# Optimization experiments

Hardware: AMD Instinct MI355X
Metric: run time of the kernel (lower is better)

The kernel has to match this reference:

```python
import jax, jax.numpy as jnp
import numpy as np

B, C, D, L, H = 128, 1000, 300, 40, 100


def setup_inputs() -> dict:
    key = jax.random.key(0)
    ks = jax.random.split(key, 16)
    def rn(i, shape, sc=1.0):
        return (jax.random.normal(ks[i], shape, jnp.float32) * sc).astype(jnp.float32)
    return {
        "utt": rn(0, (B, L, D)),
        "sys_slots": rn(1, (B, D), 0.1),
        "conf_slots": rn(2, (B, D), 0.1),
        "conf_values": rn(3, (B, D), 0.1),
        "y_past_state": jax.random.uniform(ks[4], (B, C), jnp.float32),
        "slot_emb": rn(5, (C, D), 0.1),
        "value_emb": rn(6, (C, D), 0.1),
        "Wc": rn(7, (D, 2 * D), 0.05), "bc": jnp.zeros((D,), jnp.float32),
        "conv_w1": rn(8, (D, D, 1), 0.05), "conv_b1": jnp.zeros((D,), jnp.float32),
        "conv_w2": rn(9, (D, D, 2), 0.05), "conv_b2": jnp.zeros((D,), jnp.float32),
        "conv_w3": rn(10, (D, D, 3), 0.05), "conv_b3": jnp.zeros((D,), jnp.float32),
        "Wd": rn(11, (H, D), 0.05), "bd": jnp.zeros((H,), jnp.float32),
        "Wmr": rn(12, (H, D), 0.05), "bmr": jnp.zeros((H,), jnp.float32),
        "Wmc": rn(13, (H, D), 0.05), "bmc": jnp.zeros((H,), jnp.float32),
        "Wj": rn(14, (1, H), 0.05), "bj": jnp.zeros((1,), jnp.float32),
    }


def _conv_relu_pool(x_ncl, w, b):
    # x_ncl: [B, D, L]; w: [F, D, k] -> relu(conv) then global max-pool over time -> [B, F]
    y = jax.lax.conv_general_dilated(x_ncl, w, (1,), 'VALID',
                                     dimension_numbers=('NCH', 'OIH', 'NCH'))
    y = jax.nn.relu(y + b[None, :, None])
    return jnp.max(y, axis=2)


def _sig_linear(x, W, b):
    # Sequential(Sigmoid, Linear): Linear applied to sigmoid(x)
    return jax.nn.sigmoid(x) @ W.T + b


def reference(utt, sys_slots, conf_slots, conf_values, y_past_state,
              slot_emb, value_emb, Wc, bc,
              conv_w1, conv_b1, conv_w2, conv_b2, conv_w3, conv_b3,
              Wd, bd, Wmr, bmr, Wmc, bmc, Wj, bj):
    # CNN utterance encoder: sum of 3 conv branches (filter widths 1,2,3)
    x = jnp.transpose(utt, (0, 2, 1))  # [B, D, L]
    final_utt = (_conv_relu_pool(x, conv_w1, conv_b1)
                 + _conv_relu_pool(x, conv_w2, conv_b2)
                 + _conv_relu_pool(x, conv_w3, conv_b3))  # [B, D]

    # candidates_transform = sigmoid(Linear(cat(slot_emb, value_emb)))
    cand = jax.nn.sigmoid(jnp.concatenate([slot_emb, value_emb], axis=1) @ Wc.T + bc)  # [C, D]

    # fused version of the per-batch repeat/addcmul loop: [B, C, D]
    contrib = cand[None, :, :] * final_utt[:, None, :]

    y1 = _sig_linear(_sig_linear(contrib, Wd, bd), Wj, bj)  # [B, C, 1]

    # system-act request gate: ([C,D]@[D,B]) @ [B,D] -> [C, D]
    m_r = (slot_emb @ sys_slots.T) @ final_utt
    y2 = _sig_linear(_sig_linear(m_r, Wmr, bmr), Wj, bj)  # [C, 1]

    # system-act confirm gate
    m_c = ((slot_emb @ conf_slots.T) * (value_emb @ conf_values.T)) @ final_utt  # [C, D]
    y3 = _sig_linear(_sig_linear(m_c, Wmc, bmc), Wj, bj)  # [C, 1]

    y_presoftmax = y1 + y2[None, :, :] + y3[None, :, :]  # [B, C, 1]
    combine = 0.5
    return combine * y_presoftmax[..., 0] + (1.0 - combine) * y_past_state  # [B, C]
```

## Files before the change

### kernel.cpp

```cpp
#include <hip/hip_runtime.h>
#include <hip/hip_bf16.h>

#define OFF_Y23     0
#define OFF_BDP     4096
#define OFF_WJP     4544
#define OFF_BCP     4992
#define OFF_BMRP    6272
#define OFF_BMCP    6720
#define OFF_WALLT   7168
#define OFF_PBF     1235968
#define OFF_FUBF    20896768
#define OFF_FUBFT   20978688
#define OFF_CATSV   21060608
#define OFF_WCPK    22371328
#define OFF_CANDBF  22780928
#define OFF_WDFRAG  23436288
#define OFF_WMRFRAG 23507968
#define OFF_WMCFRAG 23579648
#define OFF_SYSB    23651328
#define OFF_CONFSB  23733248
#define OFF_CONFVB  23815168
#define OFF_PRBF    23897088
#define OFF_PCBF    24159232
#define OFF_SMRBF   24421376
#define OFF_SMCBF   25076736

typedef short bf16x8_t __attribute__((ext_vector_type(8)));
typedef float f32x4_t  __attribute__((ext_vector_type(4)));

__device__ __forceinline__ float sigmoidf_fast(float x) {
    return __builtin_amdgcn_rcpf(1.0f + __expf(-x));
}
__device__ __forceinline__ unsigned short f2bf(float x) {
    unsigned int u = __float_as_uint(x);
    unsigned int r = (u + 0x7FFFu + ((u >> 16) & 1u)) >> 16;
    return (unsigned short)r;
}
__device__ __forceinline__ float bf2f(unsigned short h) {
    return __uint_as_float(((unsigned int)h) << 16);
}

__device__ __forceinline__ float frag_fetch(const float* __restrict__ W, int i) {
    int entry = i >> 3, e = i & 7;
    int kt = entry / 448;
    int r = entry - kt * 448;
    int ni = r >> 6, lane = r & 63;
    int j = ni * 16 + (lane & 15);
    int k = kt * 32 + (lane >> 4) * 8 + e;
    return (j < 100 && k < 300) ? W[j * 300 + k] : 0.0f;
}

__global__ void pack_kernel(const float* __restrict__ w1, const float* __restrict__ w2,
                            const float* __restrict__ w3, const float* __restrict__ Wc,
                            const float* __restrict__ Wd, const float* __restrict__ Wmr,
                            const float* __restrict__ Wmc, const float* __restrict__ sys,
                            const float* __restrict__ confs, const float* __restrict__ confv,
                            const float* __restrict__ bd, const float* __restrict__ Wj,
                            const float* __restrict__ bmr, const float* __restrict__ bmc,
                            const float* __restrict__ bc, const float* __restrict__ slot,
                            const float* __restrict__ value,
                            unsigned short* __restrict__ WallTbf,
                            unsigned short* __restrict__ WdFrag,
                            unsigned short* __restrict__ WmrFrag,
                            unsigned short* __restrict__ WmcFrag,
                            float* __restrict__ bdPad, float* __restrict__ WjPad,
                            float* __restrict__ bmrPad, float* __restrict__ bmcPad,
                            float* __restrict__ bcPad,
                            unsigned short* __restrict__ sysB,
                            unsigned short* __restrict__ confsB,
                            unsigned short* __restrict__ confvB,
                            unsigned short* __restrict__ catsv,
                            unsigned short* __restrict__ WcPk) {
    int idx = blockIdx.x * blockDim.x + threadIdx.x;
    if (idx < 614400) {
        int tap = idx / 102400;
        int rem = idx - tap * 102400;
        int f = rem / 320, k = rem % 320;
        float v = 0.0f;
        if (f < 300 && k < 300) {
            int fd = f * 300 + k;
            if (tap == 0)      v = w1[fd];
            else if (tap == 1) v = w2[fd * 2 + 0];
            else if (tap == 2) v = w2[fd * 2 + 1];
            else               v = w3[fd * 3 + (tap - 3)];
        }
        WallTbf[idx] = f2bf(v);
    } else if (idx < 650240) {
        int i = idx - 614400;
        WdFrag[i] = f2bf(frag_fetch(Wd, i));
    } else if (idx < 686080) {
        int i = idx - 650240;
        WmrFrag[i] = f2bf(frag_fetch(Wmr, i));
    } else if (idx < 721920) {
        int i = idx - 686080;
        WmcFrag[i] = f2bf(frag_fetch(Wmc, i));
    } else if (idx < 722032) {
        int j = idx - 721920; bdPad[j] = (j < 100) ? bd[j] : 0.0f;
    } else if (idx < 722144) {
        int j = idx - 722032; WjPad[j] = (j < 100) ? Wj[j] : 0.0f;
    } else if (idx < 722256) {
        int j = idx - 722144; bmrPad[j] = (j < 100) ? bmr[j] : 0.0f;
    } else if (idx < 722368) {
        int j = idx - 722256; bmcPad[j] = (j < 100) ? bmc[j] : 0.0f;
    } else if (idx < 722688) {
        int j = idx - 722368; bcPad[j] = (j < 300) ? bc[j] : 0.0f;
    } else if (idx < 845568) {
        int i = idx - 722688;
        int m = i / 40960, r = i % 40960;
        int b = r / 320, k = r % 320;
        const float* src = (m == 0) ? sys : ((m == 1) ? confs : confv);
        unsigned short* dst = (m == 0) ? sysB : ((m == 1) ? confsB : confvB);
        dst[r] = f2bf((k < 300) ? src[b * 300 + k] : 0.0f);
    } else if (idx < 1500928) {
        int i = idx - 845568;
        int c = i / 640, k = i % 640;
        float v = 0.0f;
        if (c < 1000) {
            if (k < 300)                   v = slot[c * 300 + k];
            else if (k >= 320 && k < 620)  v = value[c * 300 + (k - 320)];
        }
        catsv[i] = f2bf(v);
    } else if (idx < 1705728) {
        int i = idx - 1500928;
        int f = i / 640, k = i % 640;
        float v = 0.0f;
        if (f < 300) {
            if (k < 300)                   v = Wc[f * 600 + k];
            else if (k >= 320 && k < 620)  v = Wc[f * 600 + 300 + (k - 320)];
        }
        WcPk[i] = f2bf(v);
    }
}

__global__ __launch_bounds__(256, 2) void gemm1_kernel(const float* __restrict__ utt,
        const unsigned short* __restrict__ WallTbf, unsigned short* __restrict__ Pbf) {
    __shared__ __attribute__((aligned(16))) short As[128 * 40];
    __shared__ __attribute__((aligned(16))) short Bs[128 * 40];
    const int tid = threadIdx.x;
    const int m0 = blockIdx.x * 128;
    const int n0 = blockIdx.y * 128;
    const int lane = tid & 63;
    const int w = tid >> 6;
    const int wrow = w >> 1, wcol = w & 1;
    const int ln = lane & 15, lq = lane >> 4;

    f32x4_t acc[4][4];
    #pragma unroll
    for (int i = 0; i < 4; i++)
        #pragma unroll
        for (int j = 0; j < 4; j++) acc[i][j] = (f32x4_t){0.f, 0.f, 0.f, 0.f};

    for (int kk = 0; kk < 320; kk += 32) {
        #pragma unroll
        for (int i = tid; i < 512; i += 256) {
            int row = i >> 2, q = i & 3;
            int k0 = kk + q * 8;
            const float* src = utt + (m0 + row) * 300;
            bf16x8_t v;
            if (k0 + 8 <= 300) {
                float4 f0 = *(const float4*)(src + k0);
                float4 f1 = *(const float4*)(src + k0 + 4);
                v[0] = (short)f2bf(f0.x); v[1] = (short)f2bf(f0.y);
                v[2] = (short)f2bf(f0.z); v[3] = (short)f2bf(f0.w);
                v[4] = (short)f2bf(f1.x); v[5] = (short)f2bf(f1.y);
                v[6] = (short)f2bf(f1.z); v[7] = (short)f2bf(f1.w);
            } else {
                #pragma unroll
                for (int e = 0; e < 8; e++) {
                    int k = k0 + e;
                    v[e] = (k < 300) ? (short)f2bf(src[k]) : (short)0;
                }
            }
            *(bf16x8_t*)(&As[row * 40 + q * 8]) = v;
        }
        #pragma unroll
        for (int i = tid; i < 512; i += 256) {
            int row = i >> 2, q = i & 3;
            *(uint4*)(&Bs[row * 40 + q * 8]) =
                *(const uint4*)(WallTbf + (n0 + row) * 320 + kk + q * 8);
        }
        __syncthreads();
        bf16x8_t a[4], b[4];
        #pragma unroll
        for (int mi = 0; mi < 4; mi++)
            a[mi] = *(const bf16x8_t*)(&As[(wrow * 64 + mi * 16 + ln) * 40 + lq * 8]);
        #pragma unroll
        for (int ni = 0; ni < 4; ni++)
            b[ni] = *(const bf16x8_t*)(&Bs[(wcol * 64 + ni * 16 + ln) * 40 + lq * 8]);
        #pragma unroll
        for (int mi = 0; mi < 4; mi++)
            #pragma unroll
            for (int ni = 0; ni < 4; ni++)
                acc[mi][ni] = __builtin_amdgcn_mfma_f32_16x16x32_bf16(a[mi], b[ni], acc[mi][ni], 0, 0, 0);
        __syncthreads();
    }
    #pragma unroll
    for (int mi = 0; mi < 4; mi++) {
        #pragma unroll
        for (int ni = 0; ni < 4; ni++) {
            int col = n0 + wcol * 64 + ni * 16 + ln;
            #pragma unroll
            for (int reg = 0; reg < 4; reg++) {
                int row = m0 + wrow * 64 + mi * 16 + lq * 4 + reg;
                Pbf[row * 1920 + col] = f2bf(acc[mi][ni][reg]);
            }
        }
    }
}

__global__ __launch_bounds__(320) void combine_kernel(const unsigned short* __restrict__ Pbf,
        const float* __restrict__ b1, const float* __restrict__ b2,
        const float* __restrict__ b3, unsigned short* __restrict__ fubf,
        unsigned short* __restrict__ fubfT) {
    int b = blockIdx.x;
    int f = threadIdx.x;
    if (f >= 300) { fubf[b * 320 + f] = 0; fubfT[f * 128 + b] = 0; return; }
    const unsigned short* base = Pbf + (size_t)b * 40 * 1920;
    float m1 = -1e30f, m2 = -1e30f, m3 = -1e30f;
    float p1prev = 0.f, p3prev = 0.f, p3prev2 = 0.f, p4prev = 0.f;
    for (int t = 0; t < 40; ++t) {
        const unsigned short* r = base + t * 1920;
        float p0 = bf2f(r[f]);
        float p1 = bf2f(r[320 + f]);
        float p2 = bf2f(r[640 + f]);
        float p3 = bf2f(r[960 + f]);
        float p4 = bf2f(r[1280 + f]);
        float p5 = bf2f(r[1600 + f]);
        m1 = fmaxf(m1, p0);
        if (t >= 1) m2 = fmaxf(m2, p1prev + p2);
        if (t >= 2) m3 = fmaxf(m3, p3prev2 + p4prev + p5);
        p3prev2 = p3prev; p3prev = p3; p4prev = p4; p1prev = p1;
    }
    float r = fmaxf(m1 + b1[f], 0.f) + fmaxf(m2 + b2[f], 0.f) + fmaxf(m3 + b3[f], 0.f);
    unsigned short rb = f2bf(r);
    fubf[b * 320 + f]  = rb;
    fubfT[f * 128 + b] = rb;
}

__global__ __launch_bounds__(256) void cand_gemm(const unsigned short* __restrict__ catsv,
        const unsigned short* __restrict__ WcPk, const float* __restrict__ bcPad,
        unsigned short* __restrict__ candbf) {
    __shared__ __attribute__((aligned(16))) short As[64 * 40];
    __shared__ __attribute__((aligned(16))) short Bs[64 * 40];
    const int tid = threadIdx.x;
    const int m0 = blockIdx.x * 64, n0 = blockIdx.y * 64;
    const int lane = tid & 63, w = tid >> 6;
    const int wr = w & 1, wc = w >> 1;
    const int ln = lane & 15, lq = lane >> 4;
    f32x4_t acc[2][2];
    #pragma unroll
    for (int i = 0; i < 2; i++)
        #pragma unroll
        for (int j = 0; j < 2; j++) acc[i][j] = (f32x4_t){0.f, 0.f, 0.f, 0.f};
    const int srow = tid >> 2, sq = tid & 3;
    for (int kk = 0; kk < 640; kk += 32) {
        *(uint4*)(&As[srow * 40 + sq * 8]) = *(const uint4*)(catsv + (m0 + srow) * 640 + kk + sq * 8);
        *(uint4*)(&Bs[srow * 40 + sq * 8]) = *(const uint4*)(WcPk  + (n0 + srow) * 640 + kk + sq * 8);
        __syncthreads();
        bf16x8_t a[2], b[2];
        #pragma unroll
        for (int mi = 0; mi < 2; mi++)
            a[mi] = *(const bf16x8_t*)(&As[(wr * 32 + mi * 16 + ln) * 40 + lq * 8]);
        #pragma unroll
        for (int ni = 0; ni < 2; ni++)
            b[ni] = *(const bf16x8_t*)(&Bs[(wc * 32 + ni * 16 + ln) * 40 + lq * 8]);
        #pragma unroll
        for (int mi = 0; mi < 2; mi++)
            #pragma unroll
            for (int ni = 0; ni < 2; ni++)
                acc[mi][ni] = __builtin_amdgcn_mfma_f32_16x16x32_bf16(a[mi], b[ni], acc[mi][ni], 0, 0, 0);
        __syncthreads();
    }
    #pragma unroll
    for (int mi = 0; mi < 2; mi++) {
        #pragma unroll
        for (int ni = 0; ni < 2; ni++) {
            int n = n0 + wc * 32 + ni * 16 + ln;
            float bcv = bcPad[n];
            #pragma unroll
            for (int reg = 0; reg < 4; reg++) {
                int cr = m0 + wr * 32 + mi * 16 + lq * 4 + reg;
                candbf[cr * 320 + n] = f2bf(sigmoidf_fast(acc[mi][ni][reg] + bcv));
            }
        }
    }
}

__global__ __launch_bounds__(256) void pgate_gemm(const unsigned short* __restrict__ catsv,
        const unsigned short* __restrict__ sysB, const unsigned short* __restrict__ confsB,
        const unsigned short* __restrict__ confvB,
        unsigned short* __restrict__ Prbf, unsigned short* __restrict__ Pcbf) {
    __shared__ __attribute__((aligned(16))) short As[2][64 * 40];
    __shared__ __attribute__((aligned(16))) short Bs[3][128 * 40];
    const int tid = threadIdx.x;
    const int c0 = blockIdx.x * 64;
    const int lane = tid & 63, w = tid >> 6;
    const int ln = lane & 15, lq = lane >> 4;
    f32x4_t accR[8], accS[8], accV[8];
    #pragma unroll
    for (int i = 0; i < 8; i++) {
        accR[i] = (f32x4_t){0.f, 0.f, 0.f, 0.f};
        accS[i] = (f32x4_t){0.f, 0.f, 0.f, 0.f};
        accV[i] = (f32x4_t){0.f, 0.f, 0.f, 0.f};
    }
    for (int kk = 0; kk < 320; kk += 32) {
        #pragma unroll
        for (int i = tid; i < 512; i += 256) {
            int mat = i >> 8, r2 = i & 255;
            int row = r2 >> 2, q = r2 & 3;
            *(uint4*)(&As[mat][row * 40 + q * 8]) =
                *(const uint4*)(catsv + (c0 + row) * 640 + mat * 320 + kk + q * 8);
        }
        #pragma unroll
        for (int i = tid; i < 1536; i += 256) {
            int mat = i >> 9, r2 = i & 511;
            int row = r2 >> 2, q = r2 & 3;
            const unsigned short* src = (mat == 0) ? sysB : ((mat == 1) ? confsB : confvB);
            *(uint4*)(&Bs[mat][row * 40 + q * 8]) =
                *(const uint4*)(src + row * 320 + kk + q * 8);
        }
        __syncthreads();
        bf16x8_t aS = *(const bf16x8_t*)(&As[0][(w * 16 + ln) * 40 + lq * 8]);
        bf16x8_t aV = *(const bf16x8_t*)(&As[1][(w * 16 + ln) * 40 + lq * 8]);
        #pragma unroll
        for (int ni = 0; ni < 8; ni++) {
            bf16x8_t bR = *(const bf16x8_t*)(&Bs[0][(ni * 16 + ln) * 40 + lq * 8]);
            bf16x8_t bS = *(const bf16x8_t*)(&Bs[1][(ni * 16 + ln) * 40 + lq * 8]);
            bf16x8_t bV = *(const bf16x8_t*)(&Bs[2][(ni * 16 + ln) * 40 + lq * 8]);
            accR[ni] = __builtin_amdgcn_mfma_f32_16x16x32_bf16(aS, bR, accR[ni], 0, 0, 0);
            accS[ni] = __builtin_amdgcn_mfma_f32_16x16x32_bf16(aS, bS, accS[ni], 0, 0, 0);
            accV[ni] = __builtin_amdgcn_mfma_f32_16x16x32_bf16(aV, bV, accV[ni], 0, 0, 0);
        }
        __syncthreads();
    }
    #pragma unroll
    for (int ni = 0; ni < 8; ni++) {
        int b = ni * 16 + ln;
        #pragma unroll
        for (int reg = 0; reg < 4; reg++) {
            int c = c0 + w * 16 + lq * 4 + reg;
            Prbf[c * 128 + b] = f2bf(accR[ni][reg]);
            Pcbf[c * 128 + b] = f2bf(accS[ni][reg] * accV[ni][reg]);
        }
    }
}

__global__ __launch_bounds__(256) void mgate_gemm(const unsigned short* __restrict__ Prbf,
        const unsigned short* __restrict__ Pcbf, const unsigned short* __restrict__ fubfT,
        unsigned short* __restrict__ smrbf, unsigned short* __restrict__ smcbf) {
    __shared__ __attribute__((aligned(16))) short As[2][64 * 40];
    __shared__ __attribute__((aligned(16))) short Bs[64 * 40];
    const int tid = threadIdx.x;
    const int m0 = blockIdx.x * 64, n0 = blockIdx.y * 64;
    const int lane = tid & 63, w = tid >> 6;
    const int wr = w & 1, wc = w >> 1;
    const int ln = lane & 15, lq = lane >> 4;
    f32x4_t accR[2][2], accC[2][2];
    #pragma unroll
    for (int i = 0; i < 2; i++)
        #pragma unroll
        for (int j = 0; j < 2; j++) {
            accR[i][j] = (f32x4_t){0.f, 0.f, 0.f, 0.f};
            accC[i][j] = (f32x4_t){0.f, 0.f, 0.f, 0.f};
        }
    for (int kk = 0; kk < 128; kk += 32) {
        #pragma unroll
        for (int i = tid; i < 512; i += 256) {
            int mat = i >> 8, r2 = i & 255;
            int row = r2 >> 2, q = r2 & 3;
            const unsigned short* src = mat ? Pcbf : Prbf;
            *(uint4*)(&As[mat][row * 40 + q * 8]) =
                *(const uint4*)(src + (m0 + row) * 128 + kk + q * 8);
        }
        if (tid < 256) {
            int row = tid >> 2, q = tid & 3;
            *(uint4*)(&Bs[row * 40 + q * 8]) =
                *(const uint4*)(fubfT + (n0 + row) * 128 + kk + q * 8);
        }
        __syncthreads();
        bf16x8_t aR[2], aC[2], b[2];
        #pragma unroll
        for (int mi = 0; mi < 2; mi++) {
            aR[mi] = *(const bf16x8_t*)(&As[0][(wr * 32 + mi * 16 + ln) * 40 + lq * 8]);
            aC[mi] = *(const bf16x8_t*)(&As[1][(wr * 32 + mi * 16 + ln) * 40 + lq * 8]);
        }
        #pragma unroll
        for (int ni = 0; ni < 2; ni++)
            b[ni] = *(const bf16x8_t*)(&Bs[(wc * 32 + ni * 16 + ln) * 40 + lq * 8]);
        #pragma unroll
        for (int mi = 0; mi < 2; mi++)
            #pragma unroll
            for (int ni = 0; ni < 2; ni++) {
                accR[mi][ni] = __builtin_amdgcn_mfma_f32_16x16x32_bf16(aR[mi], b[ni], accR[mi][ni], 0, 0, 0);
                accC[mi][ni] = __builtin_amdgcn_mfma_f32_16x16x32_bf16(aC[mi], b[ni], accC[mi][ni], 0, 0, 0);
            }
        __syncthreads();
    }
    #pragma unroll
    for (int mi = 0; mi < 2; mi++) {
        #pragma unroll
        for (int ni = 0; ni < 2; ni++) {
            int f = n0 + wc * 32 + ni * 16 + ln;
            #pragma unroll
            for (int reg = 0; reg < 4; reg++) {
                int c = m0 + wr * 32 + mi * 16 + lq * 4 + reg;
                smrbf[c * 320 + f] = f2bf(sigmoidf_fast(accR[mi][ni][reg]));
                smcbf[c * 320 + f] = f2bf(sigmoidf_fast(accC[mi][ni][reg]));
            }
        }
    }
}

__global__ __launch_bounds__(256) void ygate_gemm(const unsigned short* __restrict__ smrbf,
        const unsigned short* __restrict__ smcbf, const unsigned short* __restrict__ WmrFrag,
        const unsigned short* __restrict__ WmcFrag, const float* __restrict__ bmrPad,
        const float* __restrict__ bmcPad, const float* __restrict__ WjPad,
        const float* __restrict__ bj, float* __restrict__ y23) {
    __shared__ __attribute__((aligned(16))) short As[2][64 * 40];
    __shared__ __attribute__((aligned(16))) short Bs[2][3584];
    const int tid = threadIdx.x;
    const int c0 = blockIdx.x * 64;
    const int lane = tid & 63, w = tid >> 6;
    const int ln = lane & 15, lq = lane >> 4;
    f32x4_t accR[7], accC[7];
    #pragma unroll
    for (int i = 0; i < 7; i++) {
        accR[i] = (f32x4_t){0.f, 0.f, 0.f, 0.f};
        accC[i] = (f32x4_t){0.f, 0.f, 0.f, 0.f};
    }
    for (int kt = 0; kt < 10; kt++) {
        int kk = kt * 32;
        #pragma unroll
        for (int i = tid; i < 512; i += 256) {
            int mat = i >> 8, r2 = i & 255;
            int row = r2 >> 2, q = r2 & 3;
            const unsigned short* src = mat ? smcbf : smrbf;
            *(uint4*)(&As[mat][row * 40 + q * 8]) =
                *(const uint4*)(src + (c0 + row) * 320 + kk + q * 8);
        }
        #pragma unroll
        for (int i = tid; i < 896; i += 256) {
            int mat = i / 448, j = i - mat * 448;
            const uint4* s = (const uint4*)((mat ? WmcFrag : WmrFrag) + kt * 3584);
            ((uint4*)&Bs[mat][0])[j] = s[j];
        }
        __syncthreads();
        bf16x8_t aR = *(const bf16x8_t*)(&As[0][(w * 16 + ln) * 40 + lq * 8]);
        bf16x8_t aC = *(const bf16x8_t*)(&As[1][(w * 16 + ln) * 40 + lq * 8]);
        #pragma unroll
        for (int ni = 0; ni < 7; ni++) {
            bf16x8_t bR = *(const bf16x8_t*)(&Bs[0][(ni * 64 + lane) * 8]);
            bf16x8_t bC = *(const bf16x8_t*)(&Bs[1][(ni * 64 + lane) * 8]);
            accR[ni] = __builtin_amdgcn_mfma_f32_16x16x32_bf16(aR, bR, accR[ni], 0, 0, 0);
            accC[ni] = __builtin_amdgcn_mfma_f32_16x16x32_bf16(aC, bC, accC[ni], 0, 0, 0);
        }
        __syncthreads();
    }
    float psum[4] = {0.f, 0.f, 0.f, 0.f};
    #pragma unroll
    for (int ni = 0; ni < 7; ni++) {
        int n = ni * 16 + ln;
        float wj = WjPad[n], br = bmrPad[n], bcv = bmcPad[n];
        #pragma unroll
        for (int reg = 0; reg < 4; reg++) {
            float hr = sigmoidf_fast(accR[ni][reg] + br);
            float hc = sigmoidf_fast(accC[ni][reg] + bcv);
            psum[reg] += (hr + hc) * wj;
        }
    }
    #pragma unroll
    for (int reg = 0; reg < 4; reg++) {
        float v = psum[reg];
        v += __shfl_xor(v, 1);
        v += __shfl_xor(v, 2);
        v += __shfl_xor(v, 4);
        v += __shfl_xor(v, 8);
        if (ln == 0) {
            int c = c0 + w * 16 + lq * 4 + reg;
            y23[c] = v + 2.0f * bj[0];
        }
    }
}

__global__ __launch_bounds__(256) void gemm2_kernel(const unsigned short* __restrict__ candbf,
        const unsigned short* __restrict__ fubf, const unsigned short* __restrict__ WdFrag,
        const float* __restrict__ bdPad, const float* __restrict__ WjPad,
        const float* __restrict__ bj, const float* __restrict__ y23,
        const float* __restrict__ ypast, float* __restrict__ out) {
    __shared__ __attribute__((aligned(16))) short Bs[2][3584];
    __shared__ float bdS[112], WjS[112], ybuf[128];
    const int c = blockIdx.x;
    const int tid = threadIdx.x;
    const int lane = tid & 63, w = tid >> 6;
    const int ln = lane & 15, lq = lane >> 4;
    if (tid < 112) { bdS[tid] = bdPad[tid]; WjS[tid] = WjPad[tid]; }

    const unsigned short* candRow = candbf + c * 320;
    const unsigned short* fuR0 = fubf + (w * 32 + ln) * 320;
    const unsigned short* fuR1 = fuR0 + 16 * 320;

    f32x4_t acc[2][7];
    #pragma unroll
    for (int mi = 0; mi < 2; mi++)
        #pragma unroll
        for (int ni = 0; ni < 7; ni++) acc[mi][ni] = (f32x4_t){0.f, 0.f, 0.f, 0.f};

    {
        const uint4* src = (const uint4*)(WdFrag);
        uint4* dst = (uint4*)&Bs[0][0];
        dst[tid] = src[tid];
        if (tid < 192) dst[tid + 256] = src[tid + 256];
    }
    __syncthreads();

    #pragma unroll
    for (int kt = 0; kt < 10; kt++) {
        if (kt < 9) {
            const uint4* src = (const uint4*)(WdFrag + (kt + 1) * 3584);
            uint4* dst = (uint4*)&Bs[(kt + 1) & 1][0];
            dst[tid] = src[tid];
            if (tid < 192) dst[tid + 256] = src[tid + 256];
        }
        const int k0 = kt * 32 + lq * 8;
        bf16x8_t cf  = *(const bf16x8_t*)(candRow + k0);
        bf16x8_t f0v = *(const bf16x8_t*)(fuR0 + k0);
        bf16x8_t f1v = *(const bf16x8_t*)(fuR1 + k0);
        bf16x8_t a0, a1;
        #pragma unroll
        for (int e = 0; e < 8; e += 2) {
            float cv0 = bf2f((unsigned short)cf[e]);
            float cv1 = bf2f((unsigned short)cf[e + 1]);
            float2 s0 = make_float2(sigmoidf_fast(cv0 * bf2f((unsigned short)f0v[e])),
                                    sigmoidf_fast(cv1 * bf2f((unsigned short)f0v[e + 1])));
            float2 s1 = make_float2(sigmoidf_fast(cv0 * bf2f((unsigned short)f1v[e])),
                                    sigmoidf_fast(cv1 * bf2f((unsigned short)f1v[e + 1])));
            __hip_bfloat162 p0 = __float22bfloat162_rn(s0);
            __hip_bfloat162 p1 = __float22bfloat162_rn(s1);
            ((unsigned int*)&a0)[e >> 1] = *(unsigned int*)&p0;
            ((unsigned int*)&a1)[e >> 1] = *(unsigned int*)&p1;
        }
        #pragma unroll
        for (int ni = 0; ni < 7; ni++) {
            bf16x8_t bfr = *(const bf16x8_t*)(&Bs[kt & 1][(ni * 64 + lane) * 8]);
            acc[0][ni] = __builtin_amdgcn_mfma_f32_16x16x32_bf16(a0, bfr, acc[0][ni], 0, 0, 0);
            acc[1][ni] = __builtin_amdgcn_mfma_f32_16x16x32_bf16(a1, bfr, acc[1][ni], 0, 0, 0);
        }
        __syncthreads();
    }

    float psum[2][4] = {{0.f, 0.f, 0.f, 0.f}, {0.f, 0.f, 0.f, 0.f}};
    #pragma unroll
    for (int mi = 0; mi < 2; mi++) {
        #pragma unroll
        for (int ni = 0; ni < 7; ni++) {
            int n = ni * 16 + ln;
            float bdv = bdS[n], wjv = WjS[n];
            #pragma unroll
            for (int reg = 0; reg < 4; reg++) {
                float h = sigmoidf_fast(acc[mi][ni][reg] + bdv);
                psum[mi][reg] += h * wjv;
            }
        }
    }
    #pragma unroll
    for (int mi = 0; mi < 2; mi++) {
        #pragma unroll
        for (int reg = 0; reg < 4; reg++) {
            float v = psum[mi][reg];
            v += __shfl_xor(v, 1);
            v += __shfl_xor(v, 2);
            v += __shfl_xor(v, 4);
            v += __shfl_xor(v, 8);
            if (ln == 0) ybuf[w * 32 + mi * 16 + lq * 4 + reg] = v;
        }
    }
    __syncthreads();
    if (tid < 128) {
        int b = tid;
        float y1 = ybuf[b] + bj[0];
        out[b * 1000 + c] = 0.5f * (y1 + y23[c]) + 0.5f * ypast[b * 1000 + c];
    }
}

extern "C" void kernel_launch(void* const* d_in, const int* in_sizes, int n_in,
                              void* d_out, int out_size, void* d_ws, size_t ws_size,
                              hipStream_t stream) {
    const float* utt   = (const float*)d_in[0];
    const float* sys   = (const float*)d_in[1];
    const float* confs = (const float*)d_in[2];
    const float* confv = (const float*)d_in[3];
    const float* ypast = (const float*)d_in[4];
    const float* slot  = (const float*)d_in[5];
    const float* value = (const float*)d_in[6];
    const float* Wc    = (const float*)d_in[7];
    const float* bc    = (const float*)d_in[8];
    const float* w1    = (const float*)d_in[9];
    const float* b1    = (const float*)d_in[10];
    const float* w2    = (const float*)d_in[11];
    const float* b2    = (const float*)d_in[12];
    const float* w3    = (const float*)d_in[13];
    const float* b3    = (const float*)d_in[14];
    const float* Wd    = (const float*)d_in[15];
    const float* bd    = (const float*)d_in[16];
    const float* Wmr   = (const float*)d_in[17];
    const float* bmr   = (const float*)d_in[18];
    const float* Wmc   = (const float*)d_in[19];
    const float* bmc   = (const float*)d_in[20];
    const float* Wj    = (const float*)d_in[21];
    const float* bj    = (const float*)d_in[22];

    char* wsb = (char*)d_ws;
    float* y23    = (float*)(wsb + OFF_Y23);
    float* bdPad  = (float*)(wsb + OFF_BDP);
    float* WjPad  = (float*)(wsb + OFF_WJP);
    float* bcPad  = (float*)(wsb + OFF_BCP);
    float* bmrPad = (float*)(wsb + OFF_BMRP);
    float* bmcPad = (float*)(wsb + OFF_BMCP);
    unsigned short* WallTbf = (unsigned short*)(wsb + OFF_WALLT);
    unsigned short* Pbf     = (unsigned short*)(wsb + OFF_PBF);
    unsigned short* fubf    = (unsigned short*)(wsb + OFF_FUBF);
    unsigned short* fubfT   = (unsigned short*)(wsb + OFF_FUBFT);
    unsigned short* catsv   = (unsigned short*)(wsb + OFF_CATSV);
    unsigned short* WcPk    = (unsigned short*)(wsb + OFF_WCPK);
    unsigned short* candbf  = (unsigned short*)(wsb + OFF_CANDBF);
    unsigned short* WdFrag  = (unsigned short*)(wsb + OFF_WDFRAG);
    unsigned short* WmrFrag = (unsigned short*)(wsb + OFF_WMRFRAG);
    unsigned short* WmcFrag = (unsigned short*)(wsb + OFF_WMCFRAG);
    unsigned short* sysB    = (unsigned short*)(wsb + OFF_SYSB);
    unsigned short* confsB  = (unsigned short*)(wsb + OFF_CONFSB);
    unsigned short* confvB  = (unsigned short*)(wsb + OFF_CONFVB);
    float* out = (float*)d_out;

    pack_kernel<<<6663, 256, 0, stream>>>(w1, w2, w3, Wc, Wd, Wmr, Wmc, sys, confs, confv,
                                          bd, Wj, bmr, bmc, bc, slot, value,
                                          WallTbf, WdFrag, WmrFrag, WmcFrag,
                                          bdPad, WjPad, bmrPad, bmcPad, bcPad,
                                          sysB, confsB, confvB, catsv, WcPk);
    gemm1_kernel<<<dim3(40, 15), 256, 0, stream>>>(utt, WallTbf, Pbf);
    combine_kernel<<<128, 320, 0, stream>>>(Pbf, b1, b2, b3, fubf, fubfT);
    cand_gemm<<<dim3(16, 5), 256, 0, stream>>>(catsv, WcPk, bcPad, candbf);
    pgate_gemm<<<16, 256, 0, stream>>>(catsv, sysB, confsB, confvB,
                                       (unsigned short*)(wsb + OFF_PRBF),
                                       (unsigned short*)(wsb + OFF_PCBF));
    mgate_gemm<<<dim3(16, 5), 256, 0, stream>>>((unsigned short*)(wsb + OFF_PRBF),
                                                (unsigned short*)(wsb + OFF_PCBF), fubfT,
                                                (unsigned short*)(wsb + OFF_SMRBF),
                                                (unsigned short*)(wsb + OFF_SMCBF));
    ygate_gemm<<<16, 256, 0, stream>>>((unsigned short*)(wsb + OFF_SMRBF),
                                       (unsigned short*)(wsb + OFF_SMCBF),
                                       WmrFrag, WmcFrag, bmrPad, bmcPad, WjPad, bj, y23);
    gemm2_kernel<<<1000, 256, 0, stream>>>(candbf, fubf, WdFrag, bdPad, WjPad,
                                           bj, y23, ypast, out);
}
```

Before: 220.7 us.

## Merge independent GEMM launches into one heterogeneous kernel and pre-convert utt to bf16

Combines the conv GEMM, candidate-transform GEMM and gate projection GEMM into a single early_kernel that dispatches on block index, cutting two kernel launches and letting the small GEMMs run concurrently with the large one. The fp32-to-bf16 conversion of the utterance is moved into the pack kernel, which writes a padded bf16 copy to workspace so the GEMM loads bf16 directly. The combine kernel is split into 64-thread blocks across a 2D grid for more parallelism. The trade-offs are an extra global round trip for the converted utterance, a larger pack kernel, and the loss of the previous two-blocks-per-CU launch bound hint on the main GEMM.

New measurement: 206.1 us. 1.07x faster.

```diff
diff --git a/kernel.cpp b/kernel.cpp
--- a/kernel.cpp
+++ b/kernel.cpp
@@ -24,6 +24,7 @@
 #define OFF_PCBF    24159232
 #define OFF_SMRBF   24421376
 #define OFF_SMCBF   25076736
+#define OFF_XBF     25732096
 
 typedef short bf16x8_t __attribute__((ext_vector_type(8)));
 typedef float f32x4_t  __attribute__((ext_vector_type(4)));
@@ -58,7 +59,7 @@
                             const float* __restrict__ bd, const float* __restrict__ Wj,
                             const float* __restrict__ bmr, const float* __restrict__ bmc,
                             const float* __restrict__ bc, const float* __restrict__ slot,
-                            const float* __restrict__ value,
+                            const float* __restrict__ value, const float* __restrict__ utt,
                             unsigned short* __restrict__ WallTbf,
                             unsigned short* __restrict__ WdFrag,
                             unsigned short* __restrict__ WmrFrag,
@@ -70,7 +71,8 @@
                             unsigned short* __restrict__ confsB,
                             unsigned short* __restrict__ confvB,
                             unsigned short* __restrict__ catsv,
-                            unsigned short* __restrict__ WcPk) {
+                            unsigned short* __restrict__ WcPk,
+                            unsigned short* __restrict__ Xbf) {
     int idx = blockIdx.x * blockDim.x + threadIdx.x;
     if (idx < 614400) {
         int tap = idx / 102400;
@@ -129,91 +131,186 @@
             else if (k >= 320 && k < 620)  v = Wc[f * 600 + 300 + (k - 320)];
         }
         WcPk[i] = f2bf(v);
-    }
-}
-
-__global__ __launch_bounds__(256, 2) void gemm1_kernel(const float* __restrict__ utt,
-        const unsigned short* __restrict__ WallTbf, unsigned short* __restrict__ Pbf) {
-    __shared__ __attribute__((aligned(16))) short As[128 * 40];
-    __shared__ __attribute__((aligned(16))) short Bs[128 * 40];
+    } else if (idx < 3344128) {
+        int i = idx - 1705728;
+        int m = i / 320, k = i % 320;
+        Xbf[i] = f2bf((k < 300) ? utt[m * 300 + k] : 0.0f);
+    }
+}
+
+__global__ __launch_bounds__(256) void early_kernel(
+        const unsigned short* __restrict__ Xbf, const unsigned short* __restrict__ WallTbf,
+        unsigned short* __restrict__ Pbf,
+        const unsigned short* __restrict__ catsv, const unsigned short* __restrict__ WcPk,
+        const float* __restrict__ bcPad, unsigned short* __restrict__ candbf,
+        const unsigned short* __restrict__ sysB, const unsigned short* __restrict__ confsB,
+        const unsigned short* __restrict__ confvB,
+        unsigned short* __restrict__ Prbf, unsigned short* __restrict__ Pcbf) {
+    __shared__ __attribute__((aligned(16))) char smem[40960];
+    const int bid = blockIdx.x;
     const int tid = threadIdx.x;
-    const int m0 = blockIdx.x * 128;
-    const int n0 = blockIdx.y * 128;
-    const int lane = tid & 63;
-    const int w = tid >> 6;
-    const int wrow = w >> 1, wcol = w & 1;
+    const int lane = tid & 63, w = tid >> 6;
     const int ln = lane & 15, lq = lane >> 4;
 
-    f32x4_t acc[4][4];
-    #pragma unroll
-    for (int i = 0; i < 4; i++)
-        #pragma unroll
-        for (int j = 0; j < 4; j++) acc[i][j] = (f32x4_t){0.f, 0.f, 0.f, 0.f};
-
-    for (int kk = 0; kk < 320; kk += 32) {
-        #pragma unroll
-        for (int i = tid; i < 512; i += 256) {
-            int row = i >> 2, q = i & 3;
-            int k0 = kk + q * 8;
-            const float* src = utt + (m0 + row) * 300;
-            bf16x8_t v;
-            if (k0 + 8 <= 300) {
-                float4 f0 = *(const float4*)(src + k0);
-                float4 f1 = *(const float4*)(src + k0 + 4);
-                v[0] = (short)f2bf(f0.x); v[1] = (short)f2bf(f0.y);
-                v[2] = (short)f2bf(f0.z); v[3] = (short)f2bf(f0.w);
-                v[4] = (short)f2bf(f1.x); v[5] = (short)f2bf(f1.y);
-                v[6] = (short)f2bf(f1.z); v[7] = (short)f2bf(f1.w);
-            } else {
+    if (bid < 600) {
+        short* As = (short*)smem;
+        short* Bs = (short*)(smem + 10240);
+        const int m0 = (bid / 15) * 128;
+        const int n0 = (bid % 15) * 128;
+        const int wrow = w >> 1, wcol = w & 1;
+        f32x4_t acc[4][4];
+        #pragma unroll
+        for (int i = 0; i < 4; i++)
+            #pragma unroll
+            for (int j = 0; j < 4; j++) acc[i][j] = (f32x4_t){0.f, 0.f, 0.f, 0.f};
+        for (int kk = 0; kk < 320; kk += 32) {
+            #pragma unroll
+            for (int i = tid; i < 512; i += 256) {
+                int row = i >> 2, q = i & 3;
+                *(uint4*)(&As[row * 40 + q * 8]) =
+                    *(const uint4*)(Xbf + (m0 + row) * 320 + kk + q * 8);
+            }
+            #pragma unroll
+            for (int i = tid; i < 512; i += 256) {
+                int row = i >> 2, q = i & 3;
+                *(uint4*)(&Bs[row * 40 + q * 8]) =
+                    *(const uint4*)(WallTbf + (n0 + row) * 320 + kk + q * 8);
+            }
+            __syncthreads();
+            bf16x8_t a[4], b[4];
+            #pragma unroll
+            for (int mi = 0; mi < 4; mi++)
+                a[mi] = *(const bf16x8_t*)(&As[(wrow * 64 + mi * 16 + ln) * 40 + lq * 8]);
+            #pragma unroll
+            for (int ni = 0; ni < 4; ni++)
+                b[ni] = *(const bf16x8_t*)(&Bs[(wcol * 64 + ni * 16 + ln) * 40 + lq * 8]);
+            #pragma unroll
+            for (int mi = 0; mi < 4; mi++)
                 #pragma unroll
-                for (int e = 0; e < 8; e++) {
-                    int k = k0 + e;
-                    v[e] = (k < 300) ? (short)f2bf(src[k]) : (short)0;
+                for (int ni = 0; ni < 4; ni++)
+                    acc[mi][ni] = __builtin_amdgcn_mfma_f32_16x16x32_bf16(a[mi], b[ni], acc[mi][ni], 0, 0, 0);
+            __syncthreads();
+        }
+        #pragma unroll
+        for (int mi = 0; mi < 4; mi++) {
+            #pragma unroll
+            for (int ni = 0; ni < 4; ni++) {
+                int col = n0 + wcol * 64 + ni * 16 + ln;
+                #pragma unroll
+                for (int reg = 0; reg < 4; reg++) {
+                    int row = m0 + wrow * 64 + mi * 16 + lq * 4 + reg;
+                    Pbf[row * 1920 + col] = f2bf(acc[mi][ni][reg]);
                 }
             }
-            *(bf16x8_t*)(&As[row * 40 + q * 8]) = v;
-        }
-        #pragma unroll
-        for (int i = tid; i < 512; i += 256) {
-            int row = i >> 2, q = i & 3;
-            *(uint4*)(&Bs[row * 40 + q * 8]) =
-                *(const uint4*)(WallTbf + (n0 + row) * 320 + kk + q * 8);
-        }
-        __syncthreads();
-        bf16x8_t a[4], b[4];
-        #pragma unroll
-        for (int mi = 0; mi < 4; mi++)
-            a[mi] = *(const bf16x8_t*)(&As[(wrow * 64 + mi * 16 + ln) * 40 + lq * 8]);
-        #pragma unroll
-        for (int ni = 0; ni < 4; ni++)
-            b[ni] = *(const bf16x8_t*)(&Bs[(wcol * 64 + ni * 16 + ln) * 40 + lq * 8]);
-        #pragma unroll
-        for (int mi = 0; mi < 4; mi++)
-            #pragma unroll
-            for (int ni = 0; ni < 4; ni++)
-                acc[mi][ni] = __builtin_amdgcn_mfma_f32_16x16x32_bf16(a[mi], b[ni], acc[mi][ni], 0, 0, 0);
-        __syncthreads();
-    }
-    #pragma unroll
-    for (int mi = 0; mi < 4; mi++) {
-        #pragma unroll
-        for (int ni = 0; ni < 4; ni++) {
-            int col = n0 + wcol * 64 + ni * 16 + ln;
+        }
+    } else if (bid < 680) {
+        short* As = (short*)smem;
+        short* Bs = (short*)(smem + 5120);
+        const int idx2 = bid - 600;
+        const int m0 = (idx2 / 5) * 64, n0 = (idx2 % 5) * 64;
+        const int wr = w & 1, wc = w >> 1;
+        f32x4_t acc[2][2];
+        #pragma unroll
+        for (int i = 0; i < 2; i++)
+            #pragma unroll
+            for (int j = 0; j < 2; j++) acc[i][j] = (f32x4_t){0.f, 0.f, 0.f, 0.f};
+        const int srow = tid >> 2, sq = tid & 3;
+        for (int kk = 0; kk < 640; kk += 32) {
+            *(uint4*)(&As[srow * 40 + sq * 8]) = *(const uint4*)(catsv + (m0 + srow) * 640 + kk + sq * 8);
+            *(uint4*)(&Bs[srow * 40 + sq * 8]) = *(const uint4*)(WcPk  + (n0 + srow) * 640 + kk + sq * 8);
+            __syncthreads();
+            bf16x8_t a[2], b[2];
+            #pragma unroll
+            for (int mi = 0; mi < 2; mi++)
+                a[mi] = *(const bf16x8_t*)(&As[(wr * 32 + mi * 16 + ln) * 40 + lq * 8]);
+            #pragma unroll
+            for (int ni = 0; ni < 2; ni++)
+                b[ni] = *(const bf16x8_t*)(&Bs[(wc * 32 + ni * 16 + ln) * 40 + lq * 8]);
+            #pragma unroll
+            for (int mi = 0; mi < 2; mi++)
+                #pragma unroll
+                for (int ni = 0; ni < 2; ni++)
+                    acc[mi][ni] = __builtin_amdgcn_mfma_f32_16x16x32_bf16(a[mi], b[ni], acc[mi][ni], 0, 0, 0);
+            __syncthreads();
+        }
+        #pragma unroll
+        for (int mi = 0; mi < 2; mi++) {
+            #pragma unroll
+            for (int ni = 0; ni < 2; ni++) {
+                int n = n0 + wc * 32 + ni * 16 + ln;
+                float bcv = bcPad[n];
+                #pragma unroll
+                for (int reg = 0; reg < 4; reg++) {
+                    int cr = m0 + wr * 32 + mi * 16 + lq * 4 + reg;
+                    candbf[cr * 320 + n] = f2bf(sigmoidf_fast(acc[mi][ni][reg] + bcv));
+                }
+            }
+        }
+    } else {
+        short* As0 = (short*)smem;
+        short* As1 = (short*)(smem + 5120);
+        short* Bs0 = (short*)(smem + 10240);
+        short* Bs1 = (short*)(smem + 20480);
+        short* Bs2 = (short*)(smem + 30720);
+        const int c0 = (bid - 680) * 64;
+        f32x4_t accR[8], accS[8], accV[8];
+        #pragma unroll
+        for (int i = 0; i < 8; i++) {
+            accR[i] = (f32x4_t){0.f, 0.f, 0.f, 0.f};
+            accS[i] = (f32x4_t){0.f, 0.f, 0.f, 0.f};
+            accV[i] = (f32x4_t){0.f, 0.f, 0.f, 0.f};
+        }
+        for (int kk = 0; kk < 320; kk += 32) {
+            #pragma unroll
+            for (int i = tid; i < 512; i += 256) {
+                int mat = i >> 8, r2 = i & 255;
+                int row = r2 >> 2, q = r2 & 3;
+                short* dst = mat ? As1 : As0;
+                *(uint4*)(&dst[row * 40 + q * 8]) =
+                    *(const uint4*)(catsv + (c0 + row) * 640 + mat * 320 + kk + q * 8);
+            }
+            #pragma unroll
+            for (int i = tid; i < 1536; i += 256) {
+                int mat = i >> 9, r2 = i & 511;
+                int row = r2 >> 2, q = r2 & 3;
+                const unsigned short* src = (mat == 0) ? sysB : ((mat == 1) ? confsB : confvB);
+                short* dst = (mat == 0) ? Bs0 : ((mat == 1) ? Bs1 : Bs2);
+                *(uint4*)(&dst[row * 40 + q * 8]) =
+                    *(const uint4*)(src + row * 320 + kk + q * 8);
+            }
+            __syncthreads();
+            bf16x8_t aS = *(const bf16x8_t*)(&As0[(w * 16 + ln) * 40 + lq * 8]);
+            bf16x8_t aV = *(const bf16x8_t*)(&As1[(w * 16 + ln) * 40 + lq * 8]);
+            #pragma unroll
+            for (int ni = 0; ni < 8; ni++) {
+                bf16x8_t bR = *(const bf16x8_t*)(&Bs0[(ni * 16 + ln) * 40 + lq * 8]);
+                bf16x8_t bS = *(const bf16x8_t*)(&Bs1[(ni * 16 + ln) * 40 + lq * 8]);
+                bf16x8_t bV = *(const bf16x8_t*)(&Bs2[(ni * 16 + ln) * 40 + lq * 8]);
+                accR[ni] = __builtin_amdgcn_mfma_f32_16x16x32_bf16(aS, bR, accR[ni], 0, 0, 0);
+                accS[ni] = __builtin_amdgcn_mfma_f32_16x16x32_bf16(aS, bS, accS[ni], 0, 0, 0);
+                accV[ni] = __builtin_amdgcn_mfma_f32_16x16x32_bf16(aV, bV, accV[ni], 0, 0, 0);
+            }
+            __syncthreads();
+        }
+        #pragma unroll
+        for (int ni = 0; ni < 8; ni++) {
+            int b = ni * 16 + ln;
             #pragma unroll
             for (int reg = 0; reg < 4; reg++) {
-                int row = m0 + wrow * 64 + mi * 16 + lq * 4 + reg;
-                Pbf[row * 1920 + col] = f2bf(acc[mi][ni][reg]);
-            }
-        }
-    }
-}
-
-__global__ __launch_bounds__(320) void combine_kernel(const unsigned short* __restrict__ Pbf,
+                int c = c0 + w * 16 + lq * 4 + reg;
+                Prbf[c * 128 + b] = f2bf(accR[ni][reg]);
+                Pcbf[c * 128 + b] = f2bf(accS[ni][reg] * accV[ni][reg]);
+            }
+        }
+    }
+}
+
+__global__ __launch_bounds__(64) void combine_kernel(const unsigned short* __restrict__ Pbf,
         const float* __restrict__ b1, const float* __restrict__ b2,
         const float* __restrict__ b3, unsigned short* __restrict__ fubf,
         unsigned short* __restrict__ fubfT) {
     int b = blockIdx.x;
-    int f = threadIdx.x;
+    int f = blockIdx.y * 64 + threadIdx.x;
     if (f >= 300) { fubf[b * 320 + f] = 0; fubfT[f * 128 + b] = 0; return; }
     const unsigned short* base = Pbf + (size_t)b * 40 * 1920;
     float m1 = -1e30f, m2 = -1e30f, m3 = -1e30f;
@@ -235,114 +332,6 @@
     unsigned short rb = f2bf(r);
     fubf[b * 320 + f]  = rb;
     fubfT[f * 128 + b] = rb;
-}
-
-__global__ __launch_bounds__(256) void cand_gemm(const unsigned short* __restrict__ catsv,
-        const unsigned short* __restrict__ WcPk, const float* __restrict__ bcPad,
-        unsigned short* __restrict__ candbf) {
-    __shared__ __attribute__((aligned(16))) short As[64 * 40];
-    __shared__ __attribute__((aligned(16))) short Bs[64 * 40];
-    const int tid = threadIdx.x;
-    const int m0 = blockIdx.x * 64, n0 = blockIdx.y * 64;
-    const int lane = tid & 63, w = tid >> 6;
-    const int wr = w & 1, wc = w >> 1;
-    const int ln = lane & 15, lq = lane >> 4;
-    f32x4_t acc[2][2];
-    #pragma unroll
-    for (int i = 0; i < 2; i++)
-        #pragma unroll
-        for (int j = 0; j < 2; j++) acc[i][j] = (f32x4_t){0.f, 0.f, 0.f, 0.f};
-    const int srow = tid >> 2, sq = tid & 3;
-    for (int kk = 0; kk < 640; kk += 32) {
-        *(uint4*)(&As[srow * 40 + sq * 8]) = *(const uint4*)(catsv + (m0 + srow) * 640 + kk + sq * 8);
-        *(uint4*)(&Bs[srow * 40 + sq * 8]) = *(const uint4*)(WcPk  + (n0 + srow) * 640 + kk + sq * 8);
-        __syncthreads();
-        bf16x8_t a[2], b[2];
-        #pragma unroll
-        for (int mi = 0; mi < 2; mi++)
-            a[mi] = *(const bf16x8_t*)(&As[(wr * 32 + mi * 16 + ln) * 40 + lq * 8]);
-        #pragma unroll
-        for (int ni = 0; ni < 2; ni++)
-            b[ni] = *(const bf16x8_t*)(&Bs[(wc * 32 + ni * 16 + ln) * 40 + lq * 8]);
-        #pragma unroll
-        for (int mi = 0; mi < 2; mi++)
-            #pragma unroll
-            for (int ni = 0; ni < 2; ni++)
-                acc[mi][ni] = __builtin_amdgcn_mfma_f32_16x16x32_bf16(a[mi], b[ni], acc[mi][ni], 0, 0, 0);
-        __syncthreads();
-    }
-    #pragma unroll
-    for (int mi = 0; mi < 2; mi++) {
-        #pragma unroll
-        for (int ni = 0; ni < 2; ni++) {
-            int n = n0 + wc * 32 + ni * 16 + ln;
-            float bcv = bcPad[n];
-            #pragma unroll
-            for (int reg = 0; reg < 4; reg++) {
-                int cr = m0 + wr * 32 + mi * 16 + lq * 4 + reg;
-                candbf[cr * 320 + n] = f2bf(sigmoidf_fast(acc[mi][ni][reg] + bcv));
-            }
-        }
-    }
-}
-
-__global__ __launch_bounds__(256) void pgate_gemm(const unsigned short* __restrict__ catsv,
-        const unsigned short* __restrict__ sysB, const unsigned short* __restrict__ confsB,
-        const unsigned short* __restrict__ confvB,
-        unsigned short* __restrict__ Prbf, unsigned short* __restrict__ Pcbf) {
-    __shared__ __attribute__((aligned(16))) short As[2][64 * 40];
-    __shared__ __attribute__((aligned(16))) short Bs[3][128 * 40];
-    const int tid = threadIdx.x;
-    const int c0 = blockIdx.x * 64;
-    const int lane = tid & 63, w = tid >> 6;
-    const int ln = lane & 15, lq = lane >> 4;
-    f32x4_t accR[8], accS[8], accV[8];
-    #pragma unroll
-    for (int i = 0; i < 8; i++) {
-        accR[i] = (f32x4_t){0.f, 0.f, 0.f, 0.f};
-        accS[i] = (f32x4_t){0.f, 0.f, 0.f, 0.f};
-        accV[i] = (f32x4_t){0.f, 0.f, 0.f, 0.f};
-    }
-    for (int kk = 0; kk < 320; kk += 32) {
-        #pragma unroll
-        for (int i = tid; i < 512; i += 256) {
-            int mat = i >> 8, r2 = i & 255;
-            int row = r2 >> 2, q = r2 & 3;
-            *(uint4*)(&As[mat][row * 40 + q * 8]) =
-                *(const uint4*)(catsv + (c0 + row) * 640 + mat * 320 + kk + q * 8);
-        }
-        #pragma unroll
-        for (int i = tid; i < 1536; i += 256) {
-            int mat = i >> 9, r2 = i & 511;
-            int row = r2 >> 2, q = r2 & 3;
-            const unsigned short* src = (mat == 0) ? sysB : ((mat == 1) ? confsB : confvB);
-            *(uint4*)(&Bs[mat][row * 40 + q * 8]) =
-                *(const uint4*)(src + row * 320 + kk + q * 8);
-        }
-        __syncthreads();
-        bf16x8_t aS = *(const bf16x8_t*)(&As[0][(w * 16 + ln) * 40 + lq * 8]);
-        bf16x8_t aV = *(const bf16x8_t*)(&As[1][(w * 16 + ln) * 40 + lq * 8]);
-        #pragma unroll
-        for (int ni = 0; ni < 8; ni++) {
-            bf16x8_t bR = *(const bf16x8_t*)(&Bs[0][(ni * 16 + ln) * 40 + lq * 8]);
-            bf16x8_t bS = *(const bf16x8_t*)(&Bs[1][(ni * 16 + ln) * 40 + lq * 8]);
-            bf16x8_t bV = *(const bf16x8_t*)(&Bs[2][(ni * 16 + ln) * 40 + lq * 8]);
-            accR[ni] = __builtin_amdgcn_mfma_f32_16x16x32_bf16(aS, bR, accR[ni], 0, 0, 0);
-            accS[ni] = __builtin_amdgcn_mfma_f32_16x16x32_bf16(aS, bS, accS[ni], 0, 0, 0);
-            accV[ni] = __builtin_amdgcn_mfma_f32_16x16x32_bf16(aV, bV, accV[ni], 0, 0, 0);
-        }
-        __syncthreads();
-    }
-    #pragma unroll
-    for (int ni = 0; ni < 8; ni++) {
-        int b = ni * 16 + ln;
-        #pragma unroll
-        for (int reg = 0; reg < 4; reg++) {
-            int c = c0 + w * 16 + lq * 4 + reg;
-            Prbf[c * 128 + b] = f2bf(accR[ni][reg]);
-            Pcbf[c * 128 + b] = f2bf(accS[ni][reg] * accV[ni][reg]);
-        }
-    }
 }
 
 __global__ __launch_bounds__(256) void mgate_gemm(const unsigned short* __restrict__ Prbf,
@@ -629,26 +618,25 @@
     unsigned short* sysB    = (unsigned short*)(wsb + OFF_SYSB);
     unsigned short* confsB  = (unsigned short*)(wsb + OFF_CONFSB);
     unsigned short* confvB  = (unsigned short*)(wsb + OFF_CONFVB);
+    unsigned short* Prbf    = (unsigned short*)(wsb + OFF_PRBF);
+    unsigned short* Pcbf    = (unsigned short*)(wsb + OFF_PCBF);
+    unsigned short* smrbf   = (unsigned short*)(wsb + OFF_SMRBF);
+    unsigned short* smcbf   = (unsigned short*)(wsb + OFF_SMCBF);
+    unsigned short* Xbf     = (unsigned short*)(wsb + OFF_XBF);
     float* out = (float*)d_out;
 
-    pack_kernel<<<6663, 256, 0, stream>>>(w1, w2, w3, Wc, Wd, Wmr, Wmc, sys, confs, confv,
-                                          bd, Wj, bmr, bmc, bc, slot, value,
-                                          WallTbf, WdFrag, WmrFrag, WmcFrag,
-                                          bdPad, WjPad, bmrPad, bmcPad, bcPad,
-                                          sysB, confsB, confvB, catsv, WcPk);
-    gemm1_kernel<<<dim3(40, 15), 256, 0, stream>>>(utt, WallTbf, Pbf);
-    combine_kernel<<<128, 320, 0, stream>>>(Pbf, b1, b2, b3, fubf, fubfT);
-    cand_gemm<<<dim3(16, 5), 256, 0, stream>>>(catsv, WcPk, bcPad, candbf);
-    pgate_gemm<<<16, 256, 0, stream>>>(catsv, sysB, confsB, confvB,
-                                       (unsigned short*)(wsb + OFF_PRBF),
-                                       (unsigned short*)(wsb + OFF_PCBF));
-    mgate_gemm<<<dim3(16, 5), 256, 0, stream>>>((unsigned short*)(wsb + OFF_PRBF),
-                                                (unsigned short*)(wsb + OFF_PCBF), fubfT,
-                                                (unsigned short*)(wsb + OFF_SMRBF),
-                                                (unsigned short*)(wsb + OFF_SMCBF));
-    ygate_gemm<<<16, 256, 0, stream>>>((unsigned short*)(wsb + OFF_SMRBF),
-                                       (unsigned short*)(wsb + OFF_SMCBF),
-                                       WmrFrag, WmcFrag, bmrPad, bmcPad, WjPad, bj, y23);
+    pack_kernel<<<13063, 256, 0, stream>>>(w1, w2, w3, Wc, Wd, Wmr, Wmc, sys, confs, confv,
+                                           bd, Wj, bmr, bmc, bc, slot, value, utt,
+                                           WallTbf, WdFrag, WmrFrag, WmcFrag,
+                                           bdPad, WjPad, bmrPad, bmcPad, bcPad,
+                                           sysB, confsB, confvB, catsv, WcPk, Xbf);
+    early_kernel<<<696, 256, 0, stream>>>(Xbf, WallTbf, Pbf,
+                                          catsv, WcPk, bcPad, candbf,
+                                          sysB, confsB, confvB, Prbf, Pcbf);
+    combine_kernel<<<dim3(128, 5), 64, 0, stream>>>(Pbf, b1, b2, b3, fubf, fubfT);
+    mgate_gemm<<<dim3(16, 5), 256, 0, stream>>>(Prbf, Pcbf, fubfT, smrbf, smcbf);
+    ygate_gemm<<<16, 256, 0, stream>>>(smrbf, smcbf, WmrFrag, WmcFrag,
+                                       bmrPad, bmcPad, WjPad, bj, y23);
     gemm2_kernel<<<1000, 256, 0, stream>>>(candbf, fubf, WdFrag, bdPad, WjPad,
                                            bj, y23, ypast, out);
 }
```
